# Kernel tuning notes

Measured on AMD Instinct MI355X. Metric: run time of the kernel, lower is better.

Reference implementation:

```python
import jax, jax.numpy as jnp
import numpy as np

B, L, D, E = 32, 2048, 1024, 2048

def setup_inputs() -> dict:
    key = jax.random.key(0)
    k1, k2, k3, k4, k5 = jax.random.split(key, 5)
    scale_s = 1.0 / np.sqrt(D)
    scale_h = 1.0 / np.sqrt(E)
    return {
        "dec_hidden": jax.random.normal(k1, (B, D), jnp.float32),
        "enc_outputs": jax.random.normal(k2, (B, L, E), jnp.float32),
        "W_s": jax.random.normal(k3, (D, D), jnp.float32) * scale_s,
        "W_h": jax.random.normal(k4, (D, E), jnp.float32) * scale_h,
        "v": jax.random.normal(k5, (D,), jnp.float32) * scale_s,
    }

def reference(dec_hidden, enc_outputs, W_s, W_h, v):
    # s: [B, D] -- projected decoder state (broadcast over src_len, no repeat)
    s = jnp.einsum('bd,ed->be', dec_hidden, W_s)
    # h: [B, L, D] -- projected encoder outputs
    h = jnp.einsum('ble,de->bld', enc_outputs, W_h)
    # additive scores: v^T tanh(s + h) -> [B, L]
    scores = jnp.einsum('bld,d->bl', jnp.tanh(s[:, None, :] + h), v)
    attn = jax.nn.softmax(scores, axis=1)
    # context: weighted sum of encoder outputs -> [B, E]
    ctx = jnp.einsum('bl,ble->be', attn, enc_outputs)
    return (ctx, attn)
```

## Files before the change

kernel.cpp:

```cpp
#include <hip/hip_runtime.h>
#include <cstdint>
#include <cstddef>

#define B_ 32
#define L_ 2048
#define D_ 1024
#define E_ 2048

typedef __attribute__((ext_vector_type(8))) short short8;
typedef __attribute__((ext_vector_type(16))) float f32x16;
typedef __attribute__((ext_vector_type(4))) unsigned int uint4v;

__device__ __forceinline__ void async_copy16(const void* g, void* l) {
  __builtin_amdgcn_global_load_lds((const __attribute__((address_space(1))) void*)g,
                                   (__attribute__((address_space(3))) void*)l, 16, 0, 0);
}

__device__ __forceinline__ unsigned int pack_bf16_2(float lo, float hi) {
  unsigned int ul = __builtin_bit_cast(unsigned int, lo) + 0x8000u;
  unsigned int uh = __builtin_bit_cast(unsigned int, hi) + 0x8000u;
  return (ul >> 16) | (uh & 0xFFFF0000u);
}

__device__ __forceinline__ unsigned int cvt_pk_bf16(float lo, float hi) {
  unsigned int r;
  asm("v_cvt_pk_bf16_f32 %0, %1, %2" : "=v"(r) : "v"(lo), "v"(hi));
  return r;
}

__device__ __forceinline__ float fast_tanh(float x) {
  float e = __expf(2.0f * x);
  return 1.0f - 2.0f / (e + 1.0f);
}

__global__ __launch_bounds__(256) void k_s(const float* __restrict__ dec,
                                           const float* __restrict__ Ws,
                                           float* __restrict__ s) {
  int wid = threadIdx.x >> 6, lane = threadIdx.x & 63;
  int out = blockIdx.x * 4 + wid;
  int b = out >> 10, i = out & 1023;
  const float* dr = dec + b * D_;
  const float* wr = Ws + (size_t)i * D_;
  float acc = 0.f;
#pragma unroll
  for (int c = 0; c < 4; ++c) {
    int d0 = c * 256 + lane * 4;
    float4 x = *(const float4*)(dr + d0);
    float4 w = *(const float4*)(wr + d0);
    acc += x.x * w.x + x.y * w.y + x.z * w.z + x.w * w.w;
  }
#pragma unroll
  for (int off = 32; off >= 1; off >>= 1) acc += __shfl_xor(acc, off, 64);
  if (lane == 0) s[out] = acc;
}

__global__ __launch_bounds__(256) void k_cvt(const float* __restrict__ src,
                                             unsigned short* __restrict__ dst) {
  size_t i = ((size_t)blockIdx.x * 256 + threadIdx.x) * 8;
  float4 a = *(const float4*)(src + i);
  float4 b = *(const float4*)(src + i + 4);
  uint4v p;
  p.x = pack_bf16_2(a.x, a.y);
  p.y = pack_bf16_2(a.z, a.w);
  p.z = pack_bf16_2(b.x, b.y);
  p.w = pack_bf16_2(b.z, b.w);
  *(uint4v*)(dst + i) = p;
}

__global__ __launch_bounds__(256, 3) void k_gemm(const float* __restrict__ enc,
                                                 const unsigned short* __restrict__ whb,
                                                 const float* __restrict__ sbias,
                                                 const float* __restrict__ vvec,
                                                 float* __restrict__ scores) {
  __shared__ alignas(16) unsigned short As[64 * 128];
  __shared__ alignas(16) unsigned short Bs[2][64 * 128];

  const int tid = threadIdx.x;
  const int wid = tid >> 6;
  const int lane = tid & 63;
  const int wm = wid >> 1;
  const int wn = wid & 1;

  const int flat = blockIdx.x;
  const int nt = (flat >> 3) & 7;
  const int mt = (flat & 7) | ((flat >> 6) << 3);
  const int m_base = mt * 128, n_base = nt * 128;
  const int b_idx = m_base >> 11;

  const int aRow = lane >> 4;
  const int aG = lane & 15;
  const float* gAr = enc + (size_t)(m_base + wid * 32 + aRow) * E_ + aG * 4;
  const int aP = aRow & 1;
  const int aUl = aP * 8 + (aG >> 1);
  const int aBy = (aG & 1) * 8;
  int aWoff[8];
#pragma unroll
  for (int i = 0; i < 8; ++i) {
    int line = wid * 16 + i * 2 + (aRow >> 1);
    aWoff[i] = line * 256 + ((aUl ^ (line & 15)) << 4) + aBy;
  }

  const int rp = lane >> 4;
  const int u0 = (lane & 15) ^ rp;
  const unsigned short* gB = whb + (size_t)n_base * E_;
  int offB[4], ldsB[4];
#pragma unroll
  for (int it = 0; it < 4; ++it) {
    int ulog = u0 ^ (it << 2);
    offB[it] = (wid * 32 + it * 8 + 2 * rp + (ulog >> 3)) * E_ + (ulog & 7) * 8;
    ldsB[it] = (wid * 16 + it * 4) * 256;
  }

  const int col = lane & 31;
  const int h = lane >> 5;
  int soff[4];
#pragma unroll
  for (int ks = 0; ks < 4; ++ks)
    soff[ks] = ((((col & 1) << 3) + ks * 2 + h) ^ ((col >> 1) & 15)) << 4;
  const char* aBase[2];
#pragma unroll
  for (int mi = 0; mi < 2; ++mi)
    aBase[mi] = (const char*)As + (wm * 32 + mi * 16 + (col >> 1)) * 256;
  const char* bBase[2];
#pragma unroll
  for (int ni = 0; ni < 2; ++ni)
    bBase[ni] = (const char*)Bs + (wn * 32 + ni * 16 + (col >> 1)) * 256;

  f32x16 acc[2][2] = {};
  float4 rAv[8];

#pragma unroll
  for (int it = 0; it < 4; ++it)
    async_copy16(gB + offB[it], (char*)Bs + ldsB[it]);
#pragma unroll
  for (int i = 0; i < 8; ++i)
    rAv[i] = *(const float4*)(gAr + (size_t)(i * 4) * E_);

  int bufOff = 0;
  for (int kk = 0; kk < E_; kk += 64) {
    uint2 qa[8];
#pragma unroll
    for (int i = 0; i < 8; ++i) {
      qa[i].x = cvt_pk_bf16(rAv[i].x, rAv[i].y);
      qa[i].y = cvt_pk_bf16(rAv[i].z, rAv[i].w);
    }
    __syncthreads();
#pragma unroll
    for (int i = 0; i < 8; ++i)
      *(uint2*)((char*)As + aWoff[i]) = qa[i];
    __syncthreads();

    if (kk + 64 < E_) {
#pragma unroll
      for (int it = 0; it < 4; ++it)
        async_copy16(gB + offB[it] + kk + 64, (char*)Bs + (bufOff ^ 16384) + ldsB[it]);
#pragma unroll
      for (int i = 0; i < 8; ++i)
        rAv[i] = *(const float4*)(gAr + (size_t)(i * 4) * E_ + kk + 64);
    }

#pragma unroll
    for (int ks = 0; ks < 4; ++ks) {
      short8 bf[2], af[2];
#pragma unroll
      for (int ni = 0; ni < 2; ++ni) bf[ni] = *(const short8*)(bBase[ni] + bufOff + soff[ks]);
#pragma unroll
      for (int mi = 0; mi < 2; ++mi) af[mi] = *(const short8*)(aBase[mi] + soff[ks]);
#pragma unroll
      for (int mi = 0; mi < 2; ++mi)
#pragma unroll
        for (int ni = 0; ni < 2; ++ni)
          acc[mi][ni] = __builtin_amdgcn_mfma_f32_32x32x16_bf16(af[mi], bf[ni], acc[mi][ni], 0, 0, 0);
    }
    bufOff ^= 16384;
  }

  float vv[2], sv[2];
#pragma unroll
  for (int ni = 0; ni < 2; ++ni) {
    int n = n_base + wn * 64 + ni * 32 + col;
    vv[ni] = vvec[n];
    sv[ni] = sbias[b_idx * D_ + n];
  }
#pragma unroll
  for (int mi = 0; mi < 2; ++mi) {
#pragma unroll
    for (int reg = 0; reg < 16; ++reg) {
      float sum = 0.f;
#pragma unroll
      for (int ni = 0; ni < 2; ++ni)
        sum += vv[ni] * fast_tanh(sv[ni] + acc[mi][ni][reg]);
      sum += __shfl_xor(sum, 1, 64);
      sum += __shfl_xor(sum, 2, 64);
      sum += __shfl_xor(sum, 4, 64);
      sum += __shfl_xor(sum, 8, 64);
      sum += __shfl_xor(sum, 16, 64);
      if (col == 0)
        atomicAdd(&scores[m_base + wm * 64 + mi * 32 + (reg & 3) + 8 * (reg >> 2) + h * 4], sum);
    }
  }
}

__global__ __launch_bounds__(256) void k_softmax(float* __restrict__ sc) {
  int b = blockIdx.x, tid = threadIdx.x;
  int lane = tid & 63, wid = tid >> 6;
  float* row = sc + (size_t)b * L_;
  float vals[8];
  float mx = -1e30f;
#pragma unroll
  for (int j = 0; j < 8; ++j) { vals[j] = row[tid + j * 256]; mx = fmaxf(mx, vals[j]); }
#pragma unroll
  for (int off = 32; off >= 1; off >>= 1) mx = fmaxf(mx, __shfl_xor(mx, off, 64));
  __shared__ float redm[4], reds[4];
  if (lane == 0) redm[wid] = mx;
  __syncthreads();
  mx = fmaxf(fmaxf(redm[0], redm[1]), fmaxf(redm[2], redm[3]));
  float sum = 0.f;
#pragma unroll
  for (int j = 0; j < 8; ++j) { vals[j] = __expf(vals[j] - mx); sum += vals[j]; }
#pragma unroll
  for (int off = 32; off >= 1; off >>= 1) sum += __shfl_xor(sum, off, 64);
  if (lane == 0) reds[wid] = sum;
  __syncthreads();
  sum = reds[0] + reds[1] + reds[2] + reds[3];
  float inv = 1.0f / sum;
#pragma unroll
  for (int j = 0; j < 8; ++j) row[tid + j * 256] = vals[j] * inv;
}

__global__ __launch_bounds__(256) void k_ctx(const float* __restrict__ enc,
                                             const float* __restrict__ attn,
                                             float* __restrict__ ctx) {
  int b = blockIdx.y;
  int lc = blockIdx.x >> 1;
  int eh = blockIdx.x & 1;
  int t = threadIdx.x;
  __shared__ float aw[64];
  if (t < 64) aw[t] = attn[(size_t)b * L_ + lc * 64 + t];
  __syncthreads();
  const float* base = enc + ((size_t)b * L_ + (size_t)lc * 64) * E_ + eh * 1024;
  float4 a0 = make_float4(0.f, 0.f, 0.f, 0.f);
#pragma unroll 4
  for (int l = 0; l < 64; ++l) {
    float w = aw[l];
    float4 x0 = *(const float4*)(base + (size_t)l * E_ + t * 4);
    a0.x += w * x0.x; a0.y += w * x0.y; a0.z += w * x0.z; a0.w += w * x0.w;
  }
  float* cb = ctx + (size_t)b * E_ + eh * 1024 + t * 4;
  atomicAdd(cb + 0, a0.x);
  atomicAdd(cb + 1, a0.y);
  atomicAdd(cb + 2, a0.z);
  atomicAdd(cb + 3, a0.w);
}

extern "C" void kernel_launch(void* const* d_in, const int* in_sizes, int n_in,
                              void* d_out, int out_size, void* d_ws, size_t ws_size,
                              hipStream_t stream) {
  const float* dec = (const float*)d_in[0];
  const float* enc = (const float*)d_in[1];
  const float* Ws  = (const float*)d_in[2];
  const float* Wh  = (const float*)d_in[3];
  const float* v   = (const float*)d_in[4];

  float* ctx  = (float*)d_out;
  float* attn = (float*)d_out + B_ * E_;

  unsigned short* whb = (unsigned short*)d_ws;
  float* sbuf = (float*)((char*)d_ws + (size_t)D_ * E_ * sizeof(unsigned short));

  hipMemsetAsync(d_out, 0, (size_t)out_size * sizeof(float), stream);

  k_s<<<dim3((B_ * D_) / 4), dim3(256), 0, stream>>>(dec, Ws, sbuf);
  k_cvt<<<dim3((D_ * E_) / (256 * 8)), dim3(256), 0, stream>>>(Wh, whb);
  k_gemm<<<dim3((B_ * L_ / 128) * (D_ / 128)), dim3(256), 0, stream>>>(enc, whb, sbuf, v, attn);
  k_softmax<<<dim3(B_), dim3(256), 0, stream>>>(attn);
  k_ctx<<<dim3(64, B_), dim3(256), 0, stream>>>(enc, attn, ctx);
}
```

Baseline: 1.090 ms.

## Replace async LDS B loads with register-staged two-deep prefetch pipeline

The GEMM kernel drops the double-buffered global_load_lds path for W_h. B tiles are now staged through registers into a single LDS buffer, and encoder rows are prefetched two k-steps ahead in alternating register sets, with explicit barriers and sched_barriers. Occupancy drops from 3 to 2 blocks per CU to leave room for the extra registers. The ctx kernel unroll also goes from 4 to 8. This trades LDS footprint and async copies for more register pressure and explicit scheduling control.

```diff
diff --git a/kernel.cpp b/kernel.cpp
--- a/kernel.cpp
+++ b/kernel.cpp
@@ -10,11 +10,6 @@
 typedef __attribute__((ext_vector_type(8))) short short8;
 typedef __attribute__((ext_vector_type(16))) float f32x16;
 typedef __attribute__((ext_vector_type(4))) unsigned int uint4v;
-
-__device__ __forceinline__ void async_copy16(const void* g, void* l) {
-  __builtin_amdgcn_global_load_lds((const __attribute__((address_space(1))) void*)g,
-                                   (__attribute__((address_space(3))) void*)l, 16, 0, 0);
-}
 
 __device__ __forceinline__ unsigned int pack_bf16_2(float lo, float hi) {
   unsigned int ul = __builtin_bit_cast(unsigned int, lo) + 0x8000u;
@@ -67,13 +62,13 @@
   *(uint4v*)(dst + i) = p;
 }
 
-__global__ __launch_bounds__(256, 3) void k_gemm(const float* __restrict__ enc,
+__global__ __launch_bounds__(256, 2) void k_gemm(const float* __restrict__ enc,
                                                  const unsigned short* __restrict__ whb,
                                                  const float* __restrict__ sbias,
                                                  const float* __restrict__ vvec,
                                                  float* __restrict__ scores) {
   __shared__ alignas(16) unsigned short As[64 * 128];
-  __shared__ alignas(16) unsigned short Bs[2][64 * 128];
+  __shared__ alignas(16) unsigned short Bs[64 * 128];
 
   const int tid = threadIdx.x;
   const int wid = tid >> 6;
@@ -90,8 +85,7 @@
   const int aRow = lane >> 4;
   const int aG = lane & 15;
   const float* gAr = enc + (size_t)(m_base + wid * 32 + aRow) * E_ + aG * 4;
-  const int aP = aRow & 1;
-  const int aUl = aP * 8 + (aG >> 1);
+  const int aUl = (aRow & 1) * 8 + (aG >> 1);
   const int aBy = (aG & 1) * 8;
   int aWoff[8];
 #pragma unroll
@@ -108,7 +102,7 @@
   for (int it = 0; it < 4; ++it) {
     int ulog = u0 ^ (it << 2);
     offB[it] = (wid * 32 + it * 8 + 2 * rp + (ulog >> 3)) * E_ + (ulog & 7) * 8;
-    ldsB[it] = (wid * 16 + it * 4) * 256;
+    ldsB[it] = (wid * 16 + it * 4) * 256 + lane * 16;
   }
 
   const int col = lane & 31;
@@ -127,53 +121,65 @@
     bBase[ni] = (const char*)Bs + (wn * 32 + ni * 16 + (col >> 1)) * 256;
 
   f32x16 acc[2][2] = {};
-  float4 rAv[8];
+  float4 rAv0[8], rAv1[8];
+  uint4v rBv[4];
 
 #pragma unroll
   for (int it = 0; it < 4; ++it)
-    async_copy16(gB + offB[it], (char*)Bs + ldsB[it]);
+    rBv[it] = *(const uint4v*)(gB + offB[it]);
 #pragma unroll
   for (int i = 0; i < 8; ++i)
-    rAv[i] = *(const float4*)(gAr + (size_t)(i * 4) * E_);
-
-  int bufOff = 0;
-  for (int kk = 0; kk < E_; kk += 64) {
-    uint2 qa[8];
-#pragma unroll
-    for (int i = 0; i < 8; ++i) {
-      qa[i].x = cvt_pk_bf16(rAv[i].x, rAv[i].y);
-      qa[i].y = cvt_pk_bf16(rAv[i].z, rAv[i].w);
-    }
-    __syncthreads();
-#pragma unroll
-    for (int i = 0; i < 8; ++i)
-      *(uint2*)((char*)As + aWoff[i]) = qa[i];
-    __syncthreads();
-
-    if (kk + 64 < E_) {
-#pragma unroll
-      for (int it = 0; it < 4; ++it)
-        async_copy16(gB + offB[it] + kk + 64, (char*)Bs + (bufOff ^ 16384) + ldsB[it]);
-#pragma unroll
-      for (int i = 0; i < 8; ++i)
-        rAv[i] = *(const float4*)(gAr + (size_t)(i * 4) * E_ + kk + 64);
-    }
-
-#pragma unroll
-    for (int ks = 0; ks < 4; ++ks) {
-      short8 bf[2], af[2];
-#pragma unroll
-      for (int ni = 0; ni < 2; ++ni) bf[ni] = *(const short8*)(bBase[ni] + bufOff + soff[ks]);
-#pragma unroll
-      for (int mi = 0; mi < 2; ++mi) af[mi] = *(const short8*)(aBase[mi] + soff[ks]);
-#pragma unroll
-      for (int mi = 0; mi < 2; ++mi)
-#pragma unroll
-        for (int ni = 0; ni < 2; ++ni)
-          acc[mi][ni] = __builtin_amdgcn_mfma_f32_32x32x16_bf16(af[mi], bf[ni], acc[mi][ni], 0, 0, 0);
-    }
-    bufOff ^= 16384;
-  }
+    rAv0[i] = *(const float4*)(gAr + (size_t)(i * 4) * E_);
+#pragma unroll
+  for (int i = 0; i < 8; ++i)
+    rAv1[i] = *(const float4*)(gAr + (size_t)(i * 4) * E_ + 64);
+
+#define GPHASE(KK, RA, DO_B, DO_A)                                          \
+  {                                                                         \
+    uint2 qa[8];                                                            \
+    _Pragma("unroll") for (int i = 0; i < 8; ++i) {                         \
+      qa[i].x = cvt_pk_bf16(RA[i].x, RA[i].y);                              \
+      qa[i].y = cvt_pk_bf16(RA[i].z, RA[i].w);                              \
+    }                                                                       \
+    __builtin_amdgcn_sched_barrier(0);                                      \
+    __builtin_amdgcn_s_barrier();         \
+    __builtin_amdgcn_sched_barrier(0);                                      \
+    _Pragma("unroll") for (int i = 0; i < 8; ++i)                           \
+      *(uint2*)((char*)As + aWoff[i]) = qa[i];                              \
+    _Pragma("unroll") for (int it = 0; it < 4; ++it)                        \
+      *(uint4v*)((char*)Bs + ldsB[it]) = rBv[it];                           \
+    if (DO_B) {                                                             \
+      _Pragma("unroll") for (int it = 0; it < 4; ++it)                      \
+        rBv[it] = *(const uint4v*)(gB + offB[it] + (KK) + 64);              \
+    }                                                                       \
+    if (DO_A) {                                                             \
+      _Pragma("unroll") for (int i = 0; i < 8; ++i)                         \
+        RA[i] = *(const float4*)(gAr + (size_t)(i * 4) * E_ + (KK) + 128);  \
+    }                                                                       \
+    asm volatile("s_waitcnt lgkmcnt(0)" ::: "memory");                      \
+    __builtin_amdgcn_sched_barrier(0);                                      \
+    __builtin_amdgcn_s_barrier();                    \
+    __builtin_amdgcn_sched_barrier(0);                                      \
+    _Pragma("unroll") for (int ks = 0; ks < 4; ++ks) {                      \
+      short8 bf[2], af[2];                                                  \
+      _Pragma("unroll") for (int ni = 0; ni < 2; ++ni)                      \
+        bf[ni] = *(const short8*)(bBase[ni] + soff[ks]);                    \
+      _Pragma("unroll") for (int mi = 0; mi < 2; ++mi)                      \
+        af[mi] = *(const short8*)(aBase[mi] + soff[ks]);                    \
+      _Pragma("unroll") for (int mi = 0; mi < 2; ++mi)                      \
+        _Pragma("unroll") for (int ni = 0; ni < 2; ++ni)                    \
+          acc[mi][ni] = __builtin_amdgcn_mfma_f32_32x32x16_bf16(            \
+              af[mi], bf[ni], acc[mi][ni], 0, 0, 0);                        \
+    }                                                                       \
+  }
+
+  for (int kk = 0; kk < 1920; kk += 128) {
+    GPHASE(kk, rAv0, true, true);
+    GPHASE(kk + 64, rAv1, true, true);
+  }
+  GPHASE(1920, rAv0, true, false);
+  GPHASE(1984, rAv1, false, false);
+#undef GPHASE
 
   float vv[2], sv[2];
 #pragma unroll
@@ -240,7 +246,7 @@
   __syncthreads();
   const float* base = enc + ((size_t)b * L_ + (size_t)lc * 64) * E_ + eh * 1024;
   float4 a0 = make_float4(0.f, 0.f, 0.f, 0.f);
-#pragma unroll 4
+#pragma unroll 8
   for (int l = 0; l < 64; ++l) {
     float w = aw[l];
     float4 x0 = *(const float4*)(base + (size_t)l * E_ + t * 4);
```

Measured after the change: 1.069 ms. Within noise of the previous version (-1.9%).
